# Performance work log

Measured on AMD Instinct MI355X. Metric: run time of the kernel, lower is better.

Reference implementation:

```python
import jax, jax.numpy as jnp
import numpy as np

B, T, D, H = 64, 1024, 256, 256

def setup_inputs() -> dict:
    key = jax.random.key(0)
    k1, k2, k3 = jax.random.split(key, 3)
    s = 1.0 / np.sqrt(H)
    return {
        "x": jax.random.normal(k1, (B, T, D), dtype=jnp.float32),
        "W_ih": jax.random.uniform(k2, (H, D), dtype=jnp.float32, minval=-s, maxval=s),
        "W_hh": jax.random.uniform(k3, (H, H), dtype=jnp.float32, minval=-s, maxval=s),
        "b_ih": jnp.zeros((H,), dtype=jnp.float32),
        "b_hh": jnp.zeros((H,), dtype=jnp.float32),
    }

def reference(x, W_ih, W_hh, b_ih, b_hh):
    # Precompute input projections for all timesteps at once (same math,
    # avoids T small GEMMs): [B, T, H]
    x_proj = jnp.einsum("btd,hd->bth", x, W_ih) + b_ih
    h0 = jnp.zeros((x.shape[0], W_hh.shape[0]), dtype=x.dtype)

    def step(h, xp_t):
        h_new = jnp.tanh(xp_t + h @ W_hh.T + b_hh)
        return h_new, h_new  # output of vanilla RNN cell is the new hidden state

    # scan over time: xp time-major [T, B, H]
    _, outs = jax.lax.scan(step, h0, jnp.swapaxes(x_proj, 0, 1))
    return jnp.swapaxes(outs, 0, 1)  # [B, T, H]
```

## Files before the change

### kernel.cpp

```cpp
#include <hip/hip_runtime.h>

#define BB 64
#define TT 1024
#define DD 256
#define HH 256
#define CH 8
#define NCH (TT / CH)

typedef float vf4 __attribute__((ext_vector_type(4)));
typedef float vf2 __attribute__((ext_vector_type(2)));
struct alignas(16) v2x2 { vf2 lo, hi; };

#define LD4(p) (*(const vf4*)(p))
#define LD2(p) (*(const vf2*)(p))
#define LDW(p) (*(const v2x2*)(p))

__device__ __forceinline__ float fast_tanh(float x) {
    float e = __expf(2.0f * x);
    return 1.0f - 2.0f / (e + 1.0f);
}

#define PKFMA(acc, aa, bb) acc = __builtin_elementwise_fma((aa), (bb), (acc))

#define DPPADD(dst, src, CTRL) {                                                   \
    int _di = __builtin_amdgcn_update_dpp(0, __float_as_int(src), CTRL, 0xF, 0xF, true); \
    dst = (src) + __int_as_float(_di); }

#define FMR(rr, bb, ss)                   \
    rr.x = fmaf((ss), (bb).x, rr.x);      \
    rr.y = fmaf((ss), (bb).y, rr.y);      \
    rr.z = fmaf((ss), (bb).z, rr.z);      \
    rr.w = fmaf((ss), (bb).w, rr.w)

#define BKb 32
#define LDP 132

__global__ __attribute__((amdgpu_flat_work_group_size(256, 256),
                          amdgpu_waves_per_eu(4, 4)))
void xproj_kernel(const float* __restrict__ x, const float* __restrict__ W_ih,
                  const float* __restrict__ b_ih, float* __restrict__ xp)
{
    __shared__ float As[BKb][LDP];
    __shared__ float Bs[BKb][LDP];

    const int tid = threadIdx.x;
    const int nb = blockIdx.x & 1;
    const int mb = blockIdx.x >> 1;
    const int m0 = mb * 128;
    const int n0 = nb * 128;

    const int sr = tid >> 3;
    const int sk = (tid & 7) * 4;

    const int tx = tid & 15;
    const int ty = tid >> 4;
    const int ma = ty * 4, mh = 64 + ty * 4;
    const int na = tx * 4, nh = 64 + tx * 4;

    vf4 ra0 = 0, ra1 = 0, ra2 = 0, ra3 = 0, ra4 = 0, ra5 = 0, ra6 = 0, ra7 = 0;
    vf4 rb0 = 0, rb1 = 0, rb2 = 0, rb3 = 0, rb4 = 0, rb5 = 0, rb6 = 0, rb7 = 0;

    for (int k0 = 0; k0 < DD; k0 += BKb) {
        #pragma unroll
        for (int g = 0; g < 4; ++g) {
            const int r = sr + g * 32;
            const vf4 v = LD4(x + (size_t)(m0 + r) * DD + k0 + sk);
            As[sk + 0][r] = v.x; As[sk + 1][r] = v.y;
            As[sk + 2][r] = v.z; As[sk + 3][r] = v.w;
        }
        #pragma unroll
        for (int g = 0; g < 4; ++g) {
            const int n = sr + g * 32;
            const vf4 v = LD4(W_ih + (size_t)(n0 + n) * DD + k0 + sk);
            Bs[sk + 0][n] = v.x; Bs[sk + 1][n] = v.y;
            Bs[sk + 2][n] = v.z; Bs[sk + 3][n] = v.w;
        }
        __syncthreads();

        #pragma unroll
        for (int kk = 0; kk < BKb; ++kk) {
            const vf4 alo = LD4(&As[kk][ma]);
            const vf4 ahi = LD4(&As[kk][mh]);
            const vf4 bl  = LD4(&Bs[kk][na]);
            const vf4 bh  = LD4(&Bs[kk][nh]);
            FMR(ra0, bl, alo.x); FMR(rb0, bh, alo.x);
            FMR(ra1, bl, alo.y); FMR(rb1, bh, alo.y);
            FMR(ra2, bl, alo.z); FMR(rb2, bh, alo.z);
            FMR(ra3, bl, alo.w); FMR(rb3, bh, alo.w);
            FMR(ra4, bl, ahi.x); FMR(rb4, bh, ahi.x);
            FMR(ra5, bl, ahi.y); FMR(rb5, bh, ahi.y);
            FMR(ra6, bl, ahi.z); FMR(rb6, bh, ahi.z);
            FMR(ra7, bl, ahi.w); FMR(rb7, bh, ahi.w);
        }
        __syncthreads();
    }

    const vf4 bia = LD4(b_ih + n0 + na);
    const vf4 bib = LD4(b_ih + n0 + nh);

    #define STORE_ROW(m, rA, rB)                                   \
        {                                                          \
            float* outp = xp + (size_t)(m0 + (m)) * HH + n0;       \
            *(vf4*)(outp + na) = rA + bia;                         \
            *(vf4*)(outp + nh) = rB + bib;                         \
        }
    STORE_ROW(ma + 0, ra0, rb0); STORE_ROW(ma + 1, ra1, rb1);
    STORE_ROW(ma + 2, ra2, rb2); STORE_ROW(ma + 3, ra3, rb3);
    STORE_ROW(mh + 0, ra4, rb4); STORE_ROW(mh + 1, ra5, rb5);
    STORE_ROW(mh + 2, ra6, rb6); STORE_ROW(mh + 3, ra7, rb7);
    #undef STORE_ROW
}

__global__ __attribute__((amdgpu_flat_work_group_size(512, 512),
                          amdgpu_waves_per_eu(2, 2)))
void rnn_kernel(const float* __restrict__ W_hh, const float* __restrict__ b_hh,
                const float* __restrict__ xpin, float* __restrict__ hout)
{
    const int tid = threadIdx.x;
    const int jg = tid >> 4;
    const int c  = tid & 15;
    const int j0 = jg * 8;
    const int jmine = j0 + (c & 7);
    const int b = blockIdx.x;

    __shared__ float hbuf[2][16 * 20];
    __shared__ float xchk[2][CH * HH];
    __shared__ float obuf[2][CH * HH];

    v2x2 w[8][4];
    #pragma unroll
    for (int r = 0; r < 8; ++r) {
        const float* wr = W_hh + (size_t)(j0 + r) * HH + c * 16;
        w[r][0] = LDW(wr + 0);  w[r][1] = LDW(wr + 4);
        w[r][2] = LDW(wr + 8);  w[r][3] = LDW(wr + 12);
    }
    const float bias = b_hh[jmine];

    asm volatile("" : "+v"(w[0][0].lo), "+v"(w[0][0].hi), "+v"(w[0][1].lo), "+v"(w[0][1].hi),
                      "+v"(w[0][2].lo), "+v"(w[0][2].hi), "+v"(w[0][3].lo), "+v"(w[0][3].hi),
                      "+v"(w[1][0].lo), "+v"(w[1][0].hi), "+v"(w[1][1].lo), "+v"(w[1][1].hi),
                      "+v"(w[1][2].lo), "+v"(w[1][2].hi), "+v"(w[1][3].lo), "+v"(w[1][3].hi));
    asm volatile("" : "+v"(w[2][0].lo), "+v"(w[2][0].hi), "+v"(w[2][1].lo), "+v"(w[2][1].hi),
                      "+v"(w[2][2].lo), "+v"(w[2][2].hi), "+v"(w[2][3].lo), "+v"(w[2][3].hi),
                      "+v"(w[3][0].lo), "+v"(w[3][0].hi), "+v"(w[3][1].lo), "+v"(w[3][1].hi),
                      "+v"(w[3][2].lo), "+v"(w[3][2].hi), "+v"(w[3][3].lo), "+v"(w[3][3].hi));
    asm volatile("" : "+v"(w[4][0].lo), "+v"(w[4][0].hi), "+v"(w[4][1].lo), "+v"(w[4][1].hi),
                      "+v"(w[4][2].lo), "+v"(w[4][2].hi), "+v"(w[4][3].lo), "+v"(w[4][3].hi),
                      "+v"(w[5][0].lo), "+v"(w[5][0].hi), "+v"(w[5][1].lo), "+v"(w[5][1].hi),
                      "+v"(w[5][2].lo), "+v"(w[5][2].hi), "+v"(w[5][3].lo), "+v"(w[5][3].hi));
    asm volatile("" : "+v"(w[6][0].lo), "+v"(w[6][0].hi), "+v"(w[6][1].lo), "+v"(w[6][1].hi),
                      "+v"(w[6][2].lo), "+v"(w[6][2].hi), "+v"(w[6][3].lo), "+v"(w[6][3].hi),
                      "+v"(w[7][0].lo), "+v"(w[7][0].hi), "+v"(w[7][1].lo), "+v"(w[7][1].hi),
                      "+v"(w[7][2].lo), "+v"(w[7][2].hi), "+v"(w[7][3].lo), "+v"(w[7][3].hi));

    const float* xbase = xpin + (size_t)b * TT * HH;
    float*       obase = hout + (size_t)b * TT * HH;
    const int haddr = ((jmine >> 4) * 20) + (jmine & 15);

    vf4 rpf = LD4(xbase + tid * 4);
    if (tid < 320) hbuf[0][tid] = 0.0f;
    *(vf4*)&xchk[0][tid * 4] = rpf;
    rpf = LD4(xbase + CH * HH + tid * 4);
    __syncthreads();

    for (int ci = 0; ci < NCH; ++ci) {
        const int cb = ci & 1;

        const float* xc = &xchk[cb][0];
        float*       ob = &obuf[cb][0];

        #pragma unroll 2
        for (int s = 0; s < CH; ++s) {
            const float xpb = xc[s * HH + jmine] + bias;

            const float* hc = &hbuf[s & 1][c * 20];
            const v2x2 h0 = LDW(hc + 0), h1 = LDW(hc + 4),
                       h2 = LDW(hc + 8), h3 = LDW(hc + 12);

            vf2 a0 = {0.f, 0.f}, a1 = {0.f, 0.f}, a2 = {0.f, 0.f}, a3 = {0.f, 0.f};
            vf2 a4 = {0.f, 0.f}, a5 = {0.f, 0.f}, a6 = {0.f, 0.f}, a7 = {0.f, 0.f};
            PKFMA(a0, w[0][0].lo, h0.lo); PKFMA(a0, w[0][0].hi, h0.hi);
            PKFMA(a0, w[0][1].lo, h1.lo); PKFMA(a0, w[0][1].hi, h1.hi);
            PKFMA(a0, w[0][2].lo, h2.lo); PKFMA(a0, w[0][2].hi, h2.hi);
            PKFMA(a0, w[0][3].lo, h3.lo); PKFMA(a0, w[0][3].hi, h3.hi);
            PKFMA(a1, w[1][0].lo, h0.lo); PKFMA(a1, w[1][0].hi, h0.hi);
            PKFMA(a1, w[1][1].lo, h1.lo); PKFMA(a1, w[1][1].hi, h1.hi);
            PKFMA(a1, w[1][2].lo, h2.lo); PKFMA(a1, w[1][2].hi, h2.hi);
            PKFMA(a1, w[1][3].lo, h3.lo); PKFMA(a1, w[1][3].hi, h3.hi);
            PKFMA(a2, w[2][0].lo, h0.lo); PKFMA(a2, w[2][0].hi, h0.hi);
            PKFMA(a2, w[2][1].lo, h1.lo); PKFMA(a2, w[2][1].hi, h1.hi);
            PKFMA(a2, w[2][2].lo, h2.lo); PKFMA(a2, w[2][2].hi, h2.hi);
            PKFMA(a2, w[2][3].lo, h3.lo); PKFMA(a2, w[2][3].hi, h3.hi);
            PKFMA(a3, w[3][0].lo, h0.lo); PKFMA(a3, w[3][0].hi, h0.hi);
            PKFMA(a3, w[3][1].lo, h1.lo); PKFMA(a3, w[3][1].hi, h1.hi);
            PKFMA(a3, w[3][2].lo, h2.lo); PKFMA(a3, w[3][2].hi, h2.hi);
            PKFMA(a3, w[3][3].lo, h3.lo); PKFMA(a3, w[3][3].hi, h3.hi);
            PKFMA(a4, w[4][0].lo, h0.lo); PKFMA(a4, w[4][0].hi, h0.hi);
            PKFMA(a4, w[4][1].lo, h1.lo); PKFMA(a4, w[4][1].hi, h1.hi);
            PKFMA(a4, w[4][2].lo, h2.lo); PKFMA(a4, w[4][2].hi, h2.hi);
            PKFMA(a4, w[4][3].lo, h3.lo); PKFMA(a4, w[4][3].hi, h3.hi);
            PKFMA(a5, w[5][0].lo, h0.lo); PKFMA(a5, w[5][0].hi, h0.hi);
            PKFMA(a5, w[5][1].lo, h1.lo); PKFMA(a5, w[5][1].hi, h1.hi);
            PKFMA(a5, w[5][2].lo, h2.lo); PKFMA(a5, w[5][2].hi, h2.hi);
            PKFMA(a5, w[5][3].lo, h3.lo); PKFMA(a5, w[5][3].hi, h3.hi);
            PKFMA(a6, w[6][0].lo, h0.lo); PKFMA(a6, w[6][0].hi, h0.hi);
            PKFMA(a6, w[6][1].lo, h1.lo); PKFMA(a6, w[6][1].hi, h1.hi);
            PKFMA(a6, w[6][2].lo, h2.lo); PKFMA(a6, w[6][2].hi, h2.hi);
            PKFMA(a6, w[6][3].lo, h3.lo); PKFMA(a6, w[6][3].hi, h3.hi);
            PKFMA(a7, w[7][0].lo, h0.lo); PKFMA(a7, w[7][0].hi, h0.hi);
            PKFMA(a7, w[7][1].lo, h1.lo); PKFMA(a7, w[7][1].hi, h1.hi);
            PKFMA(a7, w[7][2].lo, h2.lo); PKFMA(a7, w[7][2].hi, h2.hi);
            PKFMA(a7, w[7][3].lo, h3.lo); PKFMA(a7, w[7][3].hi, h3.hi);

            const float s0 = a0.x + a0.y, s1 = a1.x + a1.y,
                        s2 = a2.x + a2.y, s3 = a3.x + a3.y,
                        s4 = a4.x + a4.y, s5 = a5.x + a5.y,
                        s6 = a6.x + a6.y, s7 = a7.x + a7.y;

            float t0, t1, t2, t3, t4, t5, t6, t7;
            DPPADD(t0, s0, 0xB1); DPPADD(t1, s1, 0xB1);
            DPPADD(t2, s2, 0xB1); DPPADD(t3, s3, 0xB1);
            DPPADD(t4, s4, 0xB1); DPPADD(t5, s5, 0xB1);
            DPPADD(t6, s6, 0xB1); DPPADD(t7, s7, 0xB1);
            const float p0 = (c & 1) ? t1 : t0;
            const float p1 = (c & 1) ? t3 : t2;
            const float p2 = (c & 1) ? t5 : t4;
            const float p3 = (c & 1) ? t7 : t6;
            float u0, u1, u2, u3;
            DPPADD(u0, p0, 0x4E); DPPADD(u1, p1, 0x4E);
            DPPADD(u2, p2, 0x4E); DPPADD(u3, p3, 0x4E);
            const float v0 = (c & 2) ? u1 : u0;
            const float v1 = (c & 2) ? u3 : u2;
            float q0, q1;
            DPPADD(q0, v0, 0x124); DPPADD(q1, v1, 0x124);
            float vfin = (c & 4) ? q1 : q0;
            DPPADD(vfin, vfin, 0x128);

            if (s == CH - 1 && ci != NCH - 1) {
                *(vf4*)&xchk[cb ^ 1][tid * 4] = rpf;
            }

            const float hn = fast_tanh(vfin + xpb);
            if (c < 8) {
                hbuf[1 - (s & 1)][haddr] = hn;
                ob[s * HH + jmine] = hn;
            }
            __syncthreads();
        }

        const vf4 ov = *(const vf4*)&obuf[cb][tid * 4];
        *(vf4*)(obase + (size_t)ci * CH * HH + tid * 4) = ov;
        if (ci + 2 < NCH) {
            rpf = LD4(xbase + (size_t)(ci + 2) * CH * HH + tid * 4);
        }
    }
}

extern "C" void kernel_launch(void* const* d_in, const int* in_sizes, int n_in,
                              void* d_out, int out_size, void* d_ws, size_t ws_size,
                              hipStream_t stream) {
    const float* x    = (const float*)d_in[0];
    const float* W_ih = (const float*)d_in[1];
    const float* W_hh = (const float*)d_in[2];
    const float* b_ih = (const float*)d_in[3];
    const float* b_hh = (const float*)d_in[4];
    float* out = (float*)d_out;

    const size_t xp_bytes = (size_t)BB * TT * HH * sizeof(float);
    float* xp = (ws_size >= xp_bytes) ? (float*)d_ws : out;

    xproj_kernel<<<dim3(512 * 2), dim3(256), 0, stream>>>(x, W_ih, b_ih, xp);
    rnn_kernel<<<dim3(BB), dim3(512), 0, stream>>>(W_hh, b_hh, xp, out);
}
```

Measured before the change: 781.0 us.

## Compute input projection with split-bf16 MFMA instead of FP32 FMA GEMM

Replaces the shared-memory tiled FP32 FMA GEMM for the input projection with a matrix-core kernel. Each operand is split into bf16 high and low parts and combined with three MFMA products to approximate FP32 accuracy. Each block handles 16 rows and reloads and converts W_ih from global memory with no LDS reuse. This adds conversion work, uncoalesced scalar stores and repeated weight reads, while the recurrent kernel, which probably dominates runtime, is left unchanged.

```diff
diff --git a/kernel.cpp b/kernel.cpp
--- a/kernel.cpp
+++ b/kernel.cpp
@@ -9,10 +9,11 @@
 
 typedef float vf4 __attribute__((ext_vector_type(4)));
 typedef float vf2 __attribute__((ext_vector_type(2)));
+typedef float f32x4 __attribute__((ext_vector_type(4)));
+typedef short bf16x8 __attribute__((ext_vector_type(8)));
 struct alignas(16) v2x2 { vf2 lo, hi; };
 
 #define LD4(p) (*(const vf4*)(p))
-#define LD2(p) (*(const vf2*)(p))
 #define LDW(p) (*(const v2x2*)(p))
 
 __device__ __forceinline__ float fast_tanh(float x) {
@@ -20,95 +21,78 @@
     return 1.0f - 2.0f / (e + 1.0f);
 }
 
+__device__ __forceinline__ unsigned bf16rne(float f) {
+    unsigned u = __float_as_uint(f);
+    return (u + 0x7FFFu + ((u >> 16) & 1u)) >> 16;
+}
+
 #define PKFMA(acc, aa, bb) acc = __builtin_elementwise_fma((aa), (bb), (acc))
 
 #define DPPADD(dst, src, CTRL) {                                                   \
     int _di = __builtin_amdgcn_update_dpp(0, __float_as_int(src), CTRL, 0xF, 0xF, true); \
     dst = (src) + __int_as_float(_di); }
 
-#define FMR(rr, bb, ss)                   \
-    rr.x = fmaf((ss), (bb).x, rr.x);      \
-    rr.y = fmaf((ss), (bb).y, rr.y);      \
-    rr.z = fmaf((ss), (bb).z, rr.z);      \
-    rr.w = fmaf((ss), (bb).w, rr.w)
-
-#define BKb 32
-#define LDP 132
-
-__global__ __attribute__((amdgpu_flat_work_group_size(256, 256),
-                          amdgpu_waves_per_eu(4, 4)))
-void xproj_kernel(const float* __restrict__ x, const float* __restrict__ W_ih,
-                  const float* __restrict__ b_ih, float* __restrict__ xp)
+__global__ __launch_bounds__(256)
+void xproj_mfma(const float* __restrict__ x, const float* __restrict__ W_ih,
+                const float* __restrict__ b_ih, float* __restrict__ xp)
 {
-    __shared__ float As[BKb][LDP];
-    __shared__ float Bs[BKb][LDP];
-
-    const int tid = threadIdx.x;
-    const int nb = blockIdx.x & 1;
-    const int mb = blockIdx.x >> 1;
-    const int m0 = mb * 128;
-    const int n0 = nb * 128;
-
-    const int sr = tid >> 3;
-    const int sk = (tid & 7) * 4;
-
-    const int tx = tid & 15;
-    const int ty = tid >> 4;
-    const int ma = ty * 4, mh = 64 + ty * 4;
-    const int na = tx * 4, nh = 64 + tx * 4;
-
-    vf4 ra0 = 0, ra1 = 0, ra2 = 0, ra3 = 0, ra4 = 0, ra5 = 0, ra6 = 0, ra7 = 0;
-    vf4 rb0 = 0, rb1 = 0, rb2 = 0, rb3 = 0, rb4 = 0, rb5 = 0, rb6 = 0, rb7 = 0;
-
-    for (int k0 = 0; k0 < DD; k0 += BKb) {
+    const int tid  = threadIdx.x;
+    const int lane = tid & 63;
+    const int wv   = tid >> 6;
+    const int rrow = lane & 15;
+    const int kgrp = lane >> 4;
+    const size_t m0 = (size_t)blockIdx.x * 16;
+
+    bf16x8 xa1[8], xa2[8];
+    const float* xr = x + (m0 + rrow) * DD + kgrp * 8;
+    #pragma unroll
+    for (int kk = 0; kk < 8; ++kk) {
+        const float* p = xr + kk * 32;
+        bf16x8 s1, s2;
         #pragma unroll
-        for (int g = 0; g < 4; ++g) {
-            const int r = sr + g * 32;
-            const vf4 v = LD4(x + (size_t)(m0 + r) * DD + k0 + sk);
-            As[sk + 0][r] = v.x; As[sk + 1][r] = v.y;
-            As[sk + 2][r] = v.z; As[sk + 3][r] = v.w;
-        }
+        for (int j = 0; j < 8; ++j) {
+            const float f = p[j];
+            const unsigned r1 = bf16rne(f);
+            const float f1 = __uint_as_float(r1 << 16);
+            const unsigned r2 = bf16rne(f - f1);
+            s1[j] = (short)r1;
+            s2[j] = (short)r2;
+        }
+        xa1[kk] = s1;
+        xa2[kk] = s2;
+    }
+
+    #pragma unroll
+    for (int nt = 0; nt < 4; ++nt) {
+        const int n0 = wv * 64 + nt * 16;
+        const float* wr = W_ih + (size_t)(n0 + rrow) * DD + kgrp * 8;
+
+        f32x4 c0 = {0.f, 0.f, 0.f, 0.f}, c1 = c0, c2 = c0;
         #pragma unroll
-        for (int g = 0; g < 4; ++g) {
-            const int n = sr + g * 32;
-            const vf4 v = LD4(W_ih + (size_t)(n0 + n) * DD + k0 + sk);
-            Bs[sk + 0][n] = v.x; Bs[sk + 1][n] = v.y;
-            Bs[sk + 2][n] = v.z; Bs[sk + 3][n] = v.w;
-        }
-        __syncthreads();
-
+        for (int kk = 0; kk < 8; ++kk) {
+            const float* p = wr + kk * 32;
+            bf16x8 b1, b2;
+            #pragma unroll
+            for (int j = 0; j < 8; ++j) {
+                const float f = p[j];
+                const unsigned r1 = bf16rne(f);
+                const float f1 = __uint_as_float(r1 << 16);
+                const unsigned r2 = bf16rne(f - f1);
+                b1[j] = (short)r1;
+                b2[j] = (short)r2;
+            }
+            c0 = __builtin_amdgcn_mfma_f32_16x16x32_bf16(xa1[kk], b1, c0, 0, 0, 0);
+            c1 = __builtin_amdgcn_mfma_f32_16x16x32_bf16(xa2[kk], b1, c1, 0, 0, 0);
+            c2 = __builtin_amdgcn_mfma_f32_16x16x32_bf16(xa1[kk], b2, c2, 0, 0, 0);
+        }
+
+        const float bias = b_ih[n0 + rrow];
         #pragma unroll
-        for (int kk = 0; kk < BKb; ++kk) {
-            const vf4 alo = LD4(&As[kk][ma]);
-            const vf4 ahi = LD4(&As[kk][mh]);
-            const vf4 bl  = LD4(&Bs[kk][na]);
-            const vf4 bh  = LD4(&Bs[kk][nh]);
-            FMR(ra0, bl, alo.x); FMR(rb0, bh, alo.x);
-            FMR(ra1, bl, alo.y); FMR(rb1, bh, alo.y);
-            FMR(ra2, bl, alo.z); FMR(rb2, bh, alo.z);
-            FMR(ra3, bl, alo.w); FMR(rb3, bh, alo.w);
-            FMR(ra4, bl, ahi.x); FMR(rb4, bh, ahi.x);
-            FMR(ra5, bl, ahi.y); FMR(rb5, bh, ahi.y);
-            FMR(ra6, bl, ahi.z); FMR(rb6, bh, ahi.z);
-            FMR(ra7, bl, ahi.w); FMR(rb7, bh, ahi.w);
-        }
-        __syncthreads();
-    }
-
-    const vf4 bia = LD4(b_ih + n0 + na);
-    const vf4 bib = LD4(b_ih + n0 + nh);
-
-    #define STORE_ROW(m, rA, rB)                                   \
-        {                                                          \
-            float* outp = xp + (size_t)(m0 + (m)) * HH + n0;       \
-            *(vf4*)(outp + na) = rA + bia;                         \
-            *(vf4*)(outp + nh) = rB + bib;                         \
-        }
-    STORE_ROW(ma + 0, ra0, rb0); STORE_ROW(ma + 1, ra1, rb1);
-    STORE_ROW(ma + 2, ra2, rb2); STORE_ROW(ma + 3, ra3, rb3);
-    STORE_ROW(mh + 0, ra4, rb4); STORE_ROW(mh + 1, ra5, rb5);
-    STORE_ROW(mh + 2, ra6, rb6); STORE_ROW(mh + 3, ra7, rb7);
-    #undef STORE_ROW
+        for (int r = 0; r < 4; ++r) {
+            const int mrow = kgrp * 4 + r;
+            xp[(m0 + mrow) * HH + n0 + rrow] = c0[r] + c1[r] + c2[r] + bias;
+        }
+    }
 }
 
 __global__ __attribute__((amdgpu_flat_work_group_size(512, 512),
@@ -269,6 +253,6 @@
     const size_t xp_bytes = (size_t)BB * TT * HH * sizeof(float);
     float* xp = (ws_size >= xp_bytes) ? (float*)d_ws : out;
 
-    xproj_kernel<<<dim3(512 * 2), dim3(256), 0, stream>>>(x, W_ih, b_ih, xp);
+    xproj_mfma<<<dim3(BB * TT / 16), dim3(256), 0, stream>>>(x, W_ih, b_ih, xp);
     rnn_kernel<<<dim3(BB), dim3(512), 0, stream>>>(W_hh, b_hh, xp, out);
 }
```

After: 839.7 us. +7.5%, slower.

## Compute input projection with split-bf16 MFMA instead of fp32 FMA GEMM

Applied to the files above, without the earlier changes.

Replaces the fp32 SIMT GEMM for the input projection with a matrix-core kernel. Each fp32 value is split into high and low bf16 parts and multiplied with three bf16 MFMA products, which approximates fp32 accuracy. A small pre-kernel splits W_ih into the two bf16 arrays in workspace. This path needs extra workspace and an extra launch, slightly reduces precision, and the recurrent kernel is left unchanged, so its share of the total may limit the overall effect.

```diff
diff --git a/kernel.cpp b/kernel.cpp
--- a/kernel.cpp
+++ b/kernel.cpp
@@ -9,15 +9,22 @@
 
 typedef float vf4 __attribute__((ext_vector_type(4)));
 typedef float vf2 __attribute__((ext_vector_type(2)));
+typedef float f32x4 __attribute__((ext_vector_type(4)));
+typedef short bf16x8 __attribute__((ext_vector_type(8)));
+typedef short short4v __attribute__((ext_vector_type(4)));
 struct alignas(16) v2x2 { vf2 lo, hi; };
 
 #define LD4(p) (*(const vf4*)(p))
-#define LD2(p) (*(const vf2*)(p))
 #define LDW(p) (*(const v2x2*)(p))
 
 __device__ __forceinline__ float fast_tanh(float x) {
     float e = __expf(2.0f * x);
     return 1.0f - 2.0f / (e + 1.0f);
+}
+
+__device__ __forceinline__ unsigned bf16rne(float f) {
+    unsigned u = __float_as_uint(f);
+    return (u + 0x7FFFu + ((u >> 16) & 1u)) >> 16;
 }
 
 #define PKFMA(acc, aa, bb) acc = __builtin_elementwise_fma((aa), (bb), (acc))
@@ -31,6 +38,92 @@
     rr.y = fmaf((ss), (bb).y, rr.y);      \
     rr.z = fmaf((ss), (bb).z, rr.z);      \
     rr.w = fmaf((ss), (bb).w, rr.w)
+
+__global__ __launch_bounds__(256)
+void wsplit_kernel(const float* __restrict__ W, short* __restrict__ W1,
+                   short* __restrict__ W2)
+{
+    const int i = (blockIdx.x * 256 + threadIdx.x) * 4;
+    const vf4 v = LD4(W + i);
+    short4v s1, s2;
+    #pragma unroll
+    for (int j = 0; j < 4; ++j) {
+        const float f = v[j];
+        const unsigned r1 = bf16rne(f);
+        const float f1 = __uint_as_float(r1 << 16);
+        const unsigned r2 = bf16rne(f - f1);
+        s1[j] = (short)r1;
+        s2[j] = (short)r2;
+    }
+    *(short4v*)(W1 + i) = s1;
+    *(short4v*)(W2 + i) = s2;
+}
+
+__global__ __launch_bounds__(256)
+void xproj_mfma2(const float* __restrict__ x, const short* __restrict__ W1,
+                 const short* __restrict__ W2, const float* __restrict__ b_ih,
+                 float* __restrict__ xp)
+{
+    const int tid  = threadIdx.x;
+    const int lane = tid & 63;
+    const int wv   = tid >> 6;
+    const int rrow = lane & 15;
+    const int kgrp = lane >> 4;
+    const size_t m0 = (size_t)blockIdx.x * 16;
+
+    bf16x8 xa1[8], xa2[8];
+    const float* xr = x + (m0 + rrow) * DD + kgrp * 8;
+    #pragma unroll
+    for (int kk = 0; kk < 8; ++kk) {
+        const vf4 u0 = LD4(xr + kk * 32);
+        const vf4 u1 = LD4(xr + kk * 32 + 4);
+        bf16x8 s1, s2;
+        #pragma unroll
+        for (int j = 0; j < 4; ++j) {
+            const float f = u0[j];
+            const unsigned r1 = bf16rne(f);
+            const float f1 = __uint_as_float(r1 << 16);
+            const unsigned r2 = bf16rne(f - f1);
+            s1[j] = (short)r1;
+            s2[j] = (short)r2;
+        }
+        #pragma unroll
+        for (int j = 0; j < 4; ++j) {
+            const float f = u1[j];
+            const unsigned r1 = bf16rne(f);
+            const float f1 = __uint_as_float(r1 << 16);
+            const unsigned r2 = bf16rne(f - f1);
+            s1[4 + j] = (short)r1;
+            s2[4 + j] = (short)r2;
+        }
+        xa1[kk] = s1;
+        xa2[kk] = s2;
+    }
+
+    #pragma unroll
+    for (int nt = 0; nt < 4; ++nt) {
+        const int n0 = wv * 64 + nt * 16;
+        const short* w1r = W1 + (size_t)(n0 + rrow) * DD + kgrp * 8;
+        const short* w2r = W2 + (size_t)(n0 + rrow) * DD + kgrp * 8;
+
+        f32x4 c0 = {0.f, 0.f, 0.f, 0.f}, c1 = c0, c2 = c0;
+        #pragma unroll
+        for (int kk = 0; kk < 8; ++kk) {
+            const bf16x8 b1 = *(const bf16x8*)(w1r + kk * 32);
+            const bf16x8 b2 = *(const bf16x8*)(w2r + kk * 32);
+            c0 = __builtin_amdgcn_mfma_f32_16x16x32_bf16(xa1[kk], b1, c0, 0, 0, 0);
+            c1 = __builtin_amdgcn_mfma_f32_16x16x32_bf16(xa2[kk], b1, c1, 0, 0, 0);
+            c2 = __builtin_amdgcn_mfma_f32_16x16x32_bf16(xa1[kk], b2, c2, 0, 0, 0);
+        }
+
+        const float bias = b_ih[n0 + rrow];
+        #pragma unroll
+        for (int r = 0; r < 4; ++r) {
+            const int mrow = kgrp * 4 + r;
+            xp[(m0 + mrow) * HH + n0 + rrow] = c0[r] + c1[r] + c2[r] + bias;
+        }
+    }
+}
 
 #define BKb 32
 #define LDP 132
@@ -267,8 +360,19 @@
     float* out = (float*)d_out;
 
     const size_t xp_bytes = (size_t)BB * TT * HH * sizeof(float);
-    float* xp = (ws_size >= xp_bytes) ? (float*)d_ws : out;
-
-    xproj_kernel<<<dim3(512 * 2), dim3(256), 0, stream>>>(x, W_ih, b_ih, xp);
-    rnn_kernel<<<dim3(BB), dim3(512), 0, stream>>>(W_hh, b_hh, xp, out);
-}
+    const size_t w_shorts = (size_t)HH * DD;
+    const size_t w_bytes  = w_shorts * sizeof(short);
+
+    if (ws_size >= xp_bytes + 2 * w_bytes) {
+        float* xp = (float*)d_ws;
+        short* W1 = (short*)((char*)d_ws + xp_bytes);
+        short* W2 = W1 + w_shorts;
+        wsplit_kernel<<<dim3(64), dim3(256), 0, stream>>>(W_ih, W1, W2);
+        xproj_mfma2<<<dim3(BB * TT / 16), dim3(256), 0, stream>>>(x, W1, W2, b_ih, xp);
+        rnn_kernel<<<dim3(BB), dim3(512), 0, stream>>>(W_hh, b_hh, xp, out);
+    } else {
+        float* xp = (ws_size >= xp_bytes) ? (float*)d_ws : out;
+        xproj_kernel<<<dim3(512 * 2), dim3(256), 0, stream>>>(x, W_ih, b_ih, xp);
+        rnn_kernel<<<dim3(BB), dim3(512), 0, stream>>>(W_hh, b_hh, xp, out);
+    }
+}
```

Result: slower. 842.7 us (+7.9%).
